# Kernel tuning notes

Hardware: AMD Instinct MI355X
Metric: run time of the kernel (lower is better)

Reference implementation:

```python
import jax, jax.numpy as jnp
import numpy as np

B, L, K = 8192, 200, 9
DK, DV, H = 128, 128, 4
S = K * K
CENTER = S // 2
MASK_VAL = -1000000.0


def setup_inputs() -> dict:
    key = jax.random.key(0)
    ks = jax.random.split(key, 9)
    def lin(k, out_d, in_d):
        stdv = 1.0 / np.sqrt(in_d)
        return jax.random.uniform(k, (out_d, in_d), jnp.float32, -stdv, stdv)
    return {
        "x": jax.random.normal(ks[0], (B, L, K, K), jnp.float32),
        "Wk": lin(ks[1], DK, L), "bk": jnp.zeros((DK,), jnp.float32),
        "Wv": lin(ks[2], DV, L), "bv": jnp.zeros((DV,), jnp.float32),
        "Wq": lin(ks[3], DK, L), "bq": jnp.zeros((DK,), jnp.float32),
        "Wg": lin(ks[4], 1, DV), "bg": jnp.zeros((1,), jnp.float32),
    }


def reference(x, Wk, bk, Wv, bv, Wq, bq, Wg, bg):
    b = x.shape[0]
    # (B, L, K, K) -> (B, S, L)
    xs = x.reshape(b, L, S).transpose(0, 2, 1)
    keys = xs @ Wk.T + bk                      # (B, S, DK)
    vals = xs @ Wv.T + bv                      # (B, S, DV)
    query = xs[:, CENTER:CENTER + 1] @ Wq.T + bq  # (B, 1, DK)
    dk, dv = DK // H, DV // H
    kh = keys.reshape(b, S, H, dk)
    qh = query.reshape(b, 1, H, dk)
    # scores: (B, H, 1, S); note original divides by sqrt(DK) (full key_dim)
    scores = jnp.einsum('bqhd,bshd->bhqs', qh, kh) / np.sqrt(DK).astype(np.float32)
    scores = scores.at[..., CENTER].add(MASK_VAL)  # mask center pixel
    attn = jax.nn.softmax(scores, axis=-1)
    vh = vals.reshape(b, S, H, dv)
    # concat over heads == reshape since head splits are contiguous
    surround = jnp.einsum('bhqs,bshd->bqhd', attn, vh).reshape(b, 1, H * dv)
    central = vals[:, CENTER:CENTER + 1]       # (B, 1, DV)
    gate = jax.nn.sigmoid((central - surround) @ Wg.T + bg)  # (B, 1, 1)
    return central + gate * surround
```

## Files before the change

### kernel.cpp

```cpp
#include <hip/hip_runtime.h>
#include <hip/hip_bf16.h>


typedef __attribute__((ext_vector_type(8))) short short8;
typedef __attribute__((ext_vector_type(4))) float floatx4;

#define MASK_VAL -1000000.0f
#define SCALE 0.08838834764831845f

__device__ __forceinline__ float bf2f(unsigned short v) {
  return __uint_as_float(((unsigned int)v) << 16);
}
__device__ __forceinline__ unsigned short f2bf(float f) {
  unsigned int u = __float_as_uint(f);
  u += 0x7fffu + ((u >> 16) & 1u);
  return (unsigned short)(u >> 16);
}

__global__ __launch_bounds__(256, 3)
void fused_attn_kernel(const float* __restrict__ x,
                       const float* __restrict__ Wk,
                       const float* __restrict__ Wv, const float* __restrict__ bv,
                       const float* __restrict__ Wq, const float* __restrict__ bq,
                       const float* __restrict__ Wg, const float* __restrict__ bg,
                       float* __restrict__ out) {
  __shared__ __align__(16) unsigned short x_nat[200 * 88];
  __shared__ __align__(16) float xc[200];
  __shared__ __align__(16) float q_lds[128];
  __shared__ __align__(16) float u_l[200 * 4];
  __shared__ __align__(16) float part[4 * 21 * 16];
  __shared__ __align__(16) float scores[4 * 97];
  __shared__ __align__(16) unsigned short attn[4 * 96];
  __shared__ __align__(16) float y_t[4 * 200];
  __shared__ float red[2];

  const int tid = threadIdx.x;
  const int b = blockIdx.x;
  const float* __restrict__ xb = x + (size_t)b * 16200;

  for (int f = tid; f < 16200; f += 256) {
    int l = f / 81;
    int s = f - l * 81;
    float v = xb[f];
    x_nat[l * 88 + s] = f2bf(v);
    if (s == 40) xc[l] = v;
  }
  __syncthreads();

  if (tid < 128) {
    const float* wrow = Wq + tid * 200;
    float acc = 0.f;
#pragma unroll 5
    for (int lq = 0; lq < 50; ++lq) {
      float4 w = ((const float4*)wrow)[lq];
      float4 c = ((const float4*)xc)[lq];
      acc += w.x * c.x + w.y * c.y + w.z * c.z + w.w * c.w;
    }
    q_lds[tid] = acc + bq[tid];
  }
  __syncthreads();

  if (tid < 200) {
    float ua[4];
#pragma unroll
    for (int h = 0; h < 4; ++h) {
      float a = 0.f;
#pragma unroll 2
      for (int d4 = h * 8; d4 < h * 8 + 8; ++d4) {
        float4 qv = *(const float4*)&q_lds[d4 * 4];
        const float* wc = Wk + (d4 * 4) * 200 + tid;
        a += qv.x * wc[0] + qv.y * wc[200] + qv.z * wc[400] + qv.w * wc[600];
      }
      ua[h] = a;
    }
    *(float4*)&u_l[tid * 4] = make_float4(ua[0], ua[1], ua[2], ua[3]);
  }
  __syncthreads();

  if (tid < 84) {
    int lr = tid / 21;
    int sq = tid - lr * 21;
    float ps[16];
#pragma unroll
    for (int i = 0; i < 16; ++i) ps[i] = 0.f;
    const int lbase = lr * 50;
    for (int i = 0; i < 50; ++i) {
      int l = lbase + i;
      float4 u4 = *(const float4*)&u_l[l * 4];
      unsigned long long xx = *(const unsigned long long*)&x_nat[l * 88 + sq * 4];
      float x0 = bf2f((unsigned short)(xx));
      float x1 = bf2f((unsigned short)(xx >> 16));
      float x2 = bf2f((unsigned short)(xx >> 32));
      float x3 = bf2f((unsigned short)(xx >> 48));
      ps[0]  += x0 * u4.x; ps[1]  += x0 * u4.y; ps[2]  += x0 * u4.z; ps[3]  += x0 * u4.w;
      ps[4]  += x1 * u4.x; ps[5]  += x1 * u4.y; ps[6]  += x1 * u4.z; ps[7]  += x1 * u4.w;
      ps[8]  += x2 * u4.x; ps[9]  += x2 * u4.y; ps[10] += x2 * u4.z; ps[11] += x2 * u4.w;
      ps[12] += x3 * u4.x; ps[13] += x3 * u4.y; ps[14] += x3 * u4.z; ps[15] += x3 * u4.w;
    }
    float* pb = &part[(lr * 21 + sq) * 16];
#pragma unroll
    for (int e = 0; e < 4; ++e)
      *(float4*)&pb[e * 4] = make_float4(ps[e*4+0], ps[e*4+1], ps[e*4+2], ps[e*4+3]);
  }
  __syncthreads();

  for (int idx = tid; idx < 324; idx += 256) {
    int h = idx & 3, s = idx >> 2;
    int sq = s >> 2, e = s & 3;
    float a = 0.f;
#pragma unroll
    for (int lr = 0; lr < 4; ++lr) a += part[(lr * 21 + sq) * 16 + e * 4 + h];
    scores[h * 97 + s] = a * SCALE;
  }
  __syncthreads();

  {
    int wid = tid >> 6, lane = tid & 63;
    float v1 = scores[wid * 97 + lane];
    if (lane == 40) v1 += MASK_VAL;
    bool have2 = lane < 17;
    float v2 = have2 ? scores[wid * 97 + 64 + lane] : -3.0e38f;
    float mx = fmaxf(v1, v2);
#pragma unroll
    for (int o = 32; o >= 1; o >>= 1) mx = fmaxf(mx, __shfl_xor(mx, o, 64));
    float p1 = expf(v1 - mx);
    float p2 = have2 ? expf(v2 - mx) : 0.f;
    float sm = p1 + p2;
#pragma unroll
    for (int o = 32; o >= 1; o >>= 1) sm += __shfl_xor(sm, o, 64);
    float inv = 1.0f / sm;
    attn[wid * 96 + lane] = f2bf(p1 * inv);
    if (have2) attn[wid * 96 + 64 + lane] = f2bf(p2 * inv);
  }
  __syncthreads();

  {
    int wid = tid >> 6, lane = tid & 63;
    int g = lane >> 4, m16 = lane & 15;
    int hm = (m16 < 4) ? m16 : 0;
    for (int tile = wid; tile < 13; tile += 4) {
      floatx4 acc = {0.f, 0.f, 0.f, 0.f};
      int n = tile * 16 + m16;
      int lc = (n < 200) ? n : 199;
#pragma unroll
      for (int ks = 0; ks < 3; ++ks) {
        int k0 = ks * 32 + g * 8;
        short8 a8 = *(const short8*)&attn[hm * 96 + k0];
        short8 b8 = *(const short8*)&x_nat[lc * 88 + k0];
        if (ks == 2) {
#pragma unroll
          for (int j = 0; j < 8; ++j)
            if (k0 + j > 80) { a8[j] = 0; b8[j] = 0; }
        }
        acc = __builtin_amdgcn_mfma_f32_16x16x32_bf16(a8, b8, acc, 0, 0, 0);
      }
      if (g == 0 && n < 200) {
#pragma unroll
        for (int r = 0; r < 4; ++r) y_t[r * 200 + n] = acc[r];
      }
    }
  }
  __syncthreads();

  float central_v = 0.f, surround_v = 0.f;
  if (tid < 128) {
    int h = tid >> 5;
    const float* wrow = Wv + tid * 200;
    float ac = 0.f, as = 0.f;
#pragma unroll 5
    for (int lq = 0; lq < 50; ++lq) {
      float4 w  = ((const float4*)wrow)[lq];
      float4 c  = ((const float4*)xc)[lq];
      float4 yv = *(const float4*)&y_t[h * 200 + lq * 4];
      ac += w.x * c.x + w.y * c.y + w.z * c.z + w.w * c.w;
      as += w.x * yv.x + w.y * yv.y + w.z * yv.z + w.w * yv.w;
    }
    float bvv = bv[tid];
    central_v = ac + bvv;
    surround_v = as + bvv;
    float diff = (ac - as) * Wg[tid];
#pragma unroll
    for (int o = 32; o >= 1; o >>= 1) diff += __shfl_xor(diff, o, 64);
    if ((tid & 63) == 0) red[tid >> 6] = diff;
  }
  __syncthreads();
  if (tid < 128) {
    float z = red[0] + red[1] + bg[0];
    float gate = 1.0f / (1.0f + expf(-z));
    out[(size_t)b * 128 + tid] = central_v + gate * surround_v;
  }
}

extern "C" void kernel_launch(void* const* d_in, const int* in_sizes, int n_in,
                              void* d_out, int out_size, void* d_ws, size_t ws_size,
                              hipStream_t stream) {
  const float* x  = (const float*)d_in[0];
  const float* Wk = (const float*)d_in[1];
  const float* Wv = (const float*)d_in[3];
  const float* bv = (const float*)d_in[4];
  const float* Wq = (const float*)d_in[5];
  const float* bq = (const float*)d_in[6];
  const float* Wg = (const float*)d_in[7];
  const float* bg = (const float*)d_in[8];
  float* out = (float*)d_out;

  hipLaunchKernelGGL(fused_attn_kernel, dim3(8192), dim3(256), 0, stream,
                     x, Wk, Wv, bv, Wq, bq, Wg, bg, out);
}
```

Measured before the change: 984.8 us.

## Vectorize x staging loads and pre-transpose Wq/Wv into coalesced float4 layout

The x tile is now loaded as float4 vectors into a register buffer before being converted to bf16 into LDS, replacing scalar strided loads. A small prep kernel also rewrites Wq and Wv into an l4-major float4 layout in workspace, so adjacent threads read adjacent float4s instead of 800-byte-strided rows. The aim is better global-load coalescing and more memory-level parallelism per block. In exchange there is an extra kernel launch, a 16-entry float4 register buffer that may lower occupancy, and a fallback path used when the workspace is too small.

```diff
diff --git a/kernel.cpp b/kernel.cpp
--- a/kernel.cpp
+++ b/kernel.cpp
@@ -17,12 +17,27 @@
   return (unsigned short)(u >> 16);
 }
 
+__global__ void prep_weights(const float* __restrict__ Wq,
+                             const float* __restrict__ Wv,
+                             float4* __restrict__ wq4, float4* __restrict__ wv4) {
+  int i = blockIdx.x * 256 + threadIdx.x;
+  if (i < 6400) {
+    int l4 = i >> 7, d = i & 127;
+    const float* rq = Wq + d * 200 + l4 * 4;
+    wq4[i] = make_float4(rq[0], rq[1], rq[2], rq[3]);
+    const float* rv = Wv + d * 200 + l4 * 4;
+    wv4[i] = make_float4(rv[0], rv[1], rv[2], rv[3]);
+  }
+}
+
+template <bool USE_T4>
 __global__ __launch_bounds__(256, 3)
 void fused_attn_kernel(const float* __restrict__ x,
                        const float* __restrict__ Wk,
                        const float* __restrict__ Wv, const float* __restrict__ bv,
                        const float* __restrict__ Wq, const float* __restrict__ bq,
                        const float* __restrict__ Wg, const float* __restrict__ bg,
+                       const float4* __restrict__ wq4, const float4* __restrict__ wv4,
                        float* __restrict__ out) {
   __shared__ __align__(16) unsigned short x_nat[200 * 88];
   __shared__ __align__(16) float xc[200];
@@ -36,25 +51,51 @@
 
   const int tid = threadIdx.x;
   const int b = blockIdx.x;
-  const float* __restrict__ xb = x + (size_t)b * 16200;
-
-  for (int f = tid; f < 16200; f += 256) {
-    int l = f / 81;
-    int s = f - l * 81;
-    float v = xb[f];
-    x_nat[l * 88 + s] = f2bf(v);
-    if (s == 40) xc[l] = v;
+
+  {
+    const float4* __restrict__ x4 = (const float4*)(x + (size_t)b * 16200);
+    float4 buf[16];
+#pragma unroll
+    for (int i = 0; i < 16; ++i) {
+      int id = tid + i * 256;
+      if (id < 4050) buf[i] = x4[id];
+    }
+#pragma unroll
+    for (int i = 0; i < 16; ++i) {
+      int id = tid + i * 256;
+      if (id < 4050) {
+        int f0 = id * 4;
+#pragma unroll
+        for (int j = 0; j < 4; ++j) {
+          int fj = f0 + j;
+          int lj = fj / 81;
+          int sj = fj - lj * 81;
+          float v = (j == 0) ? buf[i].x : (j == 1) ? buf[i].y : (j == 2) ? buf[i].z : buf[i].w;
+          x_nat[lj * 88 + sj] = f2bf(v);
+          if (sj == 40) xc[lj] = v;
+        }
+      }
+    }
   }
   __syncthreads();
 
   if (tid < 128) {
-    const float* wrow = Wq + tid * 200;
     float acc = 0.f;
-#pragma unroll 5
-    for (int lq = 0; lq < 50; ++lq) {
-      float4 w = ((const float4*)wrow)[lq];
-      float4 c = ((const float4*)xc)[lq];
-      acc += w.x * c.x + w.y * c.y + w.z * c.z + w.w * c.w;
+    if (USE_T4) {
+#pragma unroll 5
+      for (int lq = 0; lq < 50; ++lq) {
+        float4 w = wq4[lq * 128 + tid];
+        float4 c = ((const float4*)xc)[lq];
+        acc += w.x * c.x + w.y * c.y + w.z * c.z + w.w * c.w;
+      }
+    } else {
+      const float* wrow = Wq + tid * 200;
+#pragma unroll 5
+      for (int lq = 0; lq < 50; ++lq) {
+        float4 w = ((const float4*)wrow)[lq];
+        float4 c = ((const float4*)xc)[lq];
+        acc += w.x * c.x + w.y * c.y + w.z * c.z + w.w * c.w;
+      }
     }
     q_lds[tid] = acc + bq[tid];
   }
@@ -165,15 +206,26 @@
   float central_v = 0.f, surround_v = 0.f;
   if (tid < 128) {
     int h = tid >> 5;
-    const float* wrow = Wv + tid * 200;
     float ac = 0.f, as = 0.f;
-#pragma unroll 5
-    for (int lq = 0; lq < 50; ++lq) {
-      float4 w  = ((const float4*)wrow)[lq];
-      float4 c  = ((const float4*)xc)[lq];
-      float4 yv = *(const float4*)&y_t[h * 200 + lq * 4];
-      ac += w.x * c.x + w.y * c.y + w.z * c.z + w.w * c.w;
-      as += w.x * yv.x + w.y * yv.y + w.z * yv.z + w.w * yv.w;
+    if (USE_T4) {
+#pragma unroll 5
+      for (int lq = 0; lq < 50; ++lq) {
+        float4 w  = wv4[lq * 128 + tid];
+        float4 c  = ((const float4*)xc)[lq];
+        float4 yv = *(const float4*)&y_t[h * 200 + lq * 4];
+        ac += w.x * c.x + w.y * c.y + w.z * c.z + w.w * c.w;
+        as += w.x * yv.x + w.y * yv.y + w.z * yv.z + w.w * yv.w;
+      }
+    } else {
+      const float* wrow = Wv + tid * 200;
+#pragma unroll 5
+      for (int lq = 0; lq < 50; ++lq) {
+        float4 w  = ((const float4*)wrow)[lq];
+        float4 c  = ((const float4*)xc)[lq];
+        float4 yv = *(const float4*)&y_t[h * 200 + lq * 4];
+        ac += w.x * c.x + w.y * c.y + w.z * c.z + w.w * c.w;
+        as += w.x * yv.x + w.y * yv.y + w.z * yv.z + w.w * yv.w;
+      }
     }
     float bvv = bv[tid];
     central_v = ac + bvv;
@@ -204,6 +256,16 @@
   const float* bg = (const float*)d_in[8];
   float* out = (float*)d_out;
 
-  hipLaunchKernelGGL(fused_attn_kernel, dim3(8192), dim3(256), 0, stream,
-                     x, Wk, Wv, bv, Wq, bq, Wg, bg, out);
-}
+  const size_t need = 2 * 6400 * sizeof(float4);
+  if (ws_size >= need) {
+    float4* wq4 = (float4*)d_ws;
+    float4* wv4 = wq4 + 6400;
+    hipLaunchKernelGGL(prep_weights, dim3(25), dim3(256), 0, stream, Wq, Wv, wq4, wv4);
+    hipLaunchKernelGGL(fused_attn_kernel<true>, dim3(8192), dim3(256), 0, stream,
+                       x, Wk, Wv, bv, Wq, bq, Wg, bg, wq4, wv4, out);
+  } else {
+    hipLaunchKernelGGL(fused_attn_kernel<false>, dim3(8192), dim3(256), 0, stream,
+                       x, Wk, Wv, bv, Wq, bq, Wg, bg, (const float4*)nullptr,
+                       (const float4*)nullptr, out);
+  }
+}
```

Result: faster. 816.5 us (-17.1%).
